# Kernel optimization log

Measured on AMD Instinct MI355X. Metric: run time of the kernel, lower is better.

## Reference

```python
import jax, jax.numpy as jnp
import numpy as np

TAU_PRE = 2.0
TAU_POST = 2.0
KH, KW = 3, 3
B, CIN, H, W = 16, 64, 66, 66
COUT = 128
HOUT, WOUT = H - KH + 1, W - KW + 1  # stride 1, padding 0


def setup_inputs() -> dict:
    key = jax.random.key(0)
    k1, k2, k3, k4, k5 = jax.random.split(key, 5)
    in_spike = jax.random.uniform(k1, (B, CIN, H, W), dtype=jnp.float32)
    out_spike = jax.random.uniform(k2, (B, COUT, HOUT, WOUT), dtype=jnp.float32)
    trace_pre = jax.random.uniform(k3, (B, CIN, H, W), dtype=jnp.float32)
    trace_post = jax.random.uniform(k4, (B, COUT, HOUT, WOUT), dtype=jnp.float32)
    weight = jax.random.normal(k5, (COUT, CIN, KH, KW), dtype=jnp.float32) * 0.05
    return {"in_spike": in_spike, "out_spike": out_spike,
            "trace_pre": trace_pre, "trace_post": trace_post, "weight": weight}


def reference(in_spike, out_spike, trace_pre, trace_post, weight):
    # Trace decay + spike accumulation (faithful to torch: tr - tr/tau + spike)
    tr_pre = trace_pre - trace_pre / TAU_PRE + in_spike    # [B,Cin,H,W]
    tr_post = trace_post - trace_post / TAU_POST + out_spike  # [B,Cout,Hout,Wout]

    rows = []
    for h in range(KH):
        cols = []
        for w in range(KW):
            pre = in_spike[:, :, h:h + HOUT, w:w + WOUT]   # [B,Cin,Hout,Wout]
            trp = tr_pre[:, :, h:h + HOUT, w:w + WOUT]     # [B,Cin,Hout,Wout]
            wk = weight[:, :, h, w]                        # [Cout,Cin]
            # sum over batch and spatial dims of outer products
            s_pre = jnp.einsum('bopq,bipq->oi', tr_post, pre)      # [Cout,Cin]
            s_post = jnp.einsum('bipq,bopq->oi', trp, out_spike)   # [Cout,Cin]
            cols.append(-wk * s_pre + wk * s_post)
        rows.append(jnp.stack(cols, axis=-1))  # [Cout,Cin,KW]
    delta_w = jnp.stack(rows, axis=-2)          # [Cout,Cin,KH,KW]
    return tr_pre, tr_post, delta_w
```

## Files before the change

### kernel.cpp

```cpp
#include <hip/hip_runtime.h>


typedef unsigned short ushort_t;
typedef unsigned int uint_t;
typedef __attribute__((ext_vector_type(8))) short short8;
typedef __attribute__((ext_vector_type(4))) float floatx4;
typedef __attribute__((ext_vector_type(2))) float floatx2;

#define N_PRE   4460544
#define N_POST  8388608
#define N_DW    73728
#define O_TRPOST 4460544
#define O_DW     12849152
#define BSLICE   4325376

#define GLDS16(g, l) __builtin_amdgcn_global_load_lds( \
    (const __attribute__((address_space(1))) void*)(g), \
    (__attribute__((address_space(3))) void*)(l), 16, 0, 0)

__device__ __forceinline__ ushort_t f2bf(float f) {
  uint_t u = __builtin_bit_cast(uint_t, f);
  u = (u + 0x7FFFu + ((u >> 16) & 1u)) >> 16;
  return (ushort_t)u;
}

__global__ void k_pre_elem(const float* __restrict__ in_sp, const float* __restrict__ tpre,
                           float* __restrict__ o_trpre) {
  int t4 = (blockIdx.x * 256 + threadIdx.x) * 4;
  floatx4 tp = *(const floatx4*)(tpre + t4);
  floatx4 is = *(const floatx4*)(in_sp + t4);
  *(floatx4*)(o_trpre + t4) = 0.5f * tp + is;
}

__global__ void k_bfill(const float* __restrict__ in_sp, const float* __restrict__ tpre,
                        ushort_t* __restrict__ B1, ushort_t* __restrict__ B2) {
  int tid = blockIdx.x * 256 + threadIdx.x;
  int row = tid >> 3, q8 = (tid & 7) * 8;
  int g = row * 66 + q8;
  float ftp[10], fin[10];
  #pragma unroll
  for (int k = 0; k < 5; ++k) {
    floatx2 a = *(const floatx2*)(tpre + g + 2 * k);
    floatx2 b = *(const floatx2*)(in_sp + g + 2 * k);
    ftp[2 * k] = a.x; ftp[2 * k + 1] = a.y;
    fin[2 * k] = b.x; fin[2 * k + 1] = b.y;
  }
  ushort_t utp[10], uin[10];
  #pragma unroll
  for (int k = 0; k < 10; ++k) { utp[k] = f2bf(ftp[k]); uin[k] = f2bf(fin[k]); }
  int dst = row * 64 + q8;
  #pragma unroll
  for (int kw = 0; kw < 3; ++kw) {
    short8 v1, v2;
    #pragma unroll
    for (int k = 0; k < 8; ++k) { v1[k] = (short)utp[kw + k]; v2[k] = (short)uin[kw + k]; }
    *(short8*)(B1 + kw * BSLICE + dst) = v1;
    *(short8*)(B2 + kw * BSLICE + dst) = v2;
  }
}

__global__ void k_post(const float* __restrict__ out_sp, const float* __restrict__ tpost,
                       float* __restrict__ o_trpost,
                       ushort_t* __restrict__ A1, ushort_t* __restrict__ A2, int write_ws) {
  int t8 = (blockIdx.x * 256 + threadIdx.x) * 8;
  floatx4 o0 = *(const floatx4*)(out_sp + t8);
  floatx4 o1 = *(const floatx4*)(out_sp + t8 + 4);
  floatx4 p0 = *(const floatx4*)(tpost + t8);
  floatx4 p1 = *(const floatx4*)(tpost + t8 + 4);
  *(floatx4*)(o_trpost + t8)     = 0.5f * p0 + o0;
  *(floatx4*)(o_trpost + t8 + 4) = 0.5f * p1 + o1;
  if (write_ws) {
    short8 va, vn;
    #pragma unroll
    for (int k = 0; k < 4; ++k) {
      va[k] = (short)f2bf(o0[k]); va[k + 4] = (short)f2bf(o1[k]);
      vn[k] = (short)f2bf(-p0[k]); vn[k + 4] = (short)f2bf(-p1[k]);
    }
    *(short8*)(A1 + t8) = va;
    *(short8*)(A2 + t8) = vn;
  }
}

__global__ __launch_bounds__(128, 3)
void k_mfma(const ushort_t* __restrict__ A1, const ushort_t* __restrict__ A2,
            const ushort_t* __restrict__ B1, const ushort_t* __restrict__ B2,
            float* __restrict__ partials) {
  __shared__ short LA[8192];
  __shared__ short LB[8192];

  const int oh = blockIdx.y, e = blockIdx.z;
  const int kh = e / 3, kw = e - kh * 3;
  const int t = threadIdx.x, w = t >> 6, l = t & 63;
  const int quad = l >> 4, l16 = l & 15;
  const int wo = w * 32;

  const int lrow = l >> 3;
  const int s_sw = (l & 7) ^ (lrow & 7);
  const int aoff_lane = lrow * 4096 + s_sw * 8;
  const int boff_lane = lrow * 4224 + s_sw * 8;

  const ushort_t* PA = (w == 0) ? A1 : A2;
  const ushort_t* PB = ((w == 0) ? B1 : B2) + kw * BSLICE;
  short* la = LA + w * 4096;
  short* lb = LB + w * 4096;

  floatx4 acc[2][4] = {};

  for (int rr = 0; rr < 16; ++rr) {
    const int r = blockIdx.x * 16 + rr;
    const int b = r >> 6, p = r & 63;
    const ushort_t* ga = PA + b * 524288 + oh * 262144 + p * 64 + aoff_lane;
    const ushort_t* gb = PB + b * 270336 + (p + kh) * 64 + boff_lane;

    __syncthreads();
    #pragma unroll
    for (int j = 0; j < 8; ++j) {
      GLDS16(ga + j * 32768, la + j * 512);
      GLDS16(gb + j * 33792, lb + j * 512);
    }
    __syncthreads();

    #pragma unroll
    for (int ks = 0; ks < 2; ++ks) {
      const int s0 = ks * 4 + quad;
      const int o0 = wo + l16, o1 = wo + 16 + l16;
      const int ca0 = (o0 * 8 + (s0 ^ (o0 & 7))) * 8;
      const int ca1 = (o1 * 8 + (s0 ^ (o1 & 7))) * 8;
      short8 a00 = *(const short8*)&LA[ca0];
      short8 a10 = *(const short8*)&LA[4096 + ca0];
      short8 a01 = *(const short8*)&LA[ca1];
      short8 a11 = *(const short8*)&LA[4096 + ca1];
      #pragma unroll
      for (int nt = 0; nt < 4; ++nt) {
        const int i = nt * 16 + l16;
        const int cb = (i * 8 + (s0 ^ (i & 7))) * 8;
        short8 b0 = *(const short8*)&LB[cb];
        short8 b1 = *(const short8*)&LB[4096 + cb];
        acc[0][nt] = __builtin_amdgcn_mfma_f32_16x16x32_bf16(a00, b0, acc[0][nt], 0, 0, 0);
        acc[0][nt] = __builtin_amdgcn_mfma_f32_16x16x32_bf16(a10, b1, acc[0][nt], 0, 0, 0);
        acc[1][nt] = __builtin_amdgcn_mfma_f32_16x16x32_bf16(a01, b0, acc[1][nt], 0, 0, 0);
        acc[1][nt] = __builtin_amdgcn_mfma_f32_16x16x32_bf16(a11, b1, acc[1][nt], 0, 0, 0);
      }
    }
  }

  float* slice = partials + (size_t)((e * 64 + blockIdx.x) * 2 + oh) * 4096;
  #pragma unroll
  for (int mt = 0; mt < 2; ++mt)
    #pragma unroll
    for (int nt = 0; nt < 4; ++nt)
      #pragma unroll
      for (int rg = 0; rg < 4; ++rg) {
        int o = wo + mt * 16 + quad * 4 + rg;
        int i = nt * 16 + l16;
        slice[o * 64 + i] = acc[mt][nt][rg];
      }
}

__global__ void k_finalize(const float* __restrict__ partials,
                           const float* __restrict__ weight, float* __restrict__ dw) {
  int tid = blockIdx.x * 256 + threadIdx.x;
  int e = tid >> 13, oi = tid & 8191;
  int o = oi >> 6, i = oi & 63;
  int ohh = o >> 6, ol = o & 63;
  const float* pp = partials + (size_t)e * 524288 + ohh * 4096 + ol * 64 + i;
  float s = 0.f;
  #pragma unroll 8
  for (int x = 0; x < 64; ++x) s += pp[x * 8192];
  int wi = (o * 64 + i) * 9 + e;
  dw[wi] = 0.5f * weight[wi] * s;
}

__global__ void k_naive(const float* __restrict__ out_sp, const float* __restrict__ tpost,
                        const float* __restrict__ tpre, const float* __restrict__ in_sp,
                        const float* __restrict__ weight, float* __restrict__ dw) {
  int tid = blockIdx.x * 256 + threadIdx.x;
  int e = tid >> 13, oi = tid & 8191;
  int o = oi >> 6, i = oi & 63;
  int kh = e / 3, kw = e - kh * 3;
  float acc = 0.f;
  for (int b = 0; b < 16; ++b)
    for (int p = 0; p < 64; ++p) {
      const float* ga = out_sp + ((b * 128 + o) * 64 + p) * 64;
      const float* gn = tpost + ((b * 128 + o) * 64 + p) * 64;
      const float* gb = tpre + ((b * 64 + i) * 66 + p + kh) * 66 + kw;
      const float* gm = in_sp + ((b * 64 + i) * 66 + p + kh) * 66 + kw;
      for (int q = 0; q < 64; ++q) acc += ga[q] * gb[q] - gn[q] * gm[q];
    }
  int wi = (o * 64 + i) * 9 + kh * 3 + kw;
  dw[wi] = 0.5f * weight[wi] * acc;
}

extern "C" void kernel_launch(void* const* d_in, const int* in_sizes, int n_in,
                              void* d_out, int out_size, void* d_ws, size_t ws_size,
                              hipStream_t stream) {
  const float* in_sp  = (const float*)d_in[0];
  const float* out_sp = (const float*)d_in[1];
  const float* tpre   = (const float*)d_in[2];
  const float* tpost  = (const float*)d_in[3];
  const float* weight = (const float*)d_in[4];
  float* out = (float*)d_out;
  float* o_trpre  = out;
  float* o_trpost = out + O_TRPOST;
  float* o_dw     = out + O_DW;

  const size_t WS_NEED = 104333312;
  const int use_mfma = (ws_size >= WS_NEED) ? 1 : 0;
  ushort_t* A1 = (ushort_t*)d_ws;
  ushort_t* A2 = A1 + 8388608;
  ushort_t* B1 = A2 + 8388608;
  ushort_t* B2 = B1 + 3 * BSLICE;
  float* partials = (float*)(B2 + 3 * BSLICE);

  k_pre_elem<<<N_PRE / 4 / 256, 256, 0, stream>>>(in_sp, tpre, o_trpre);
  k_post<<<N_POST / 8 / 256, 256, 0, stream>>>(out_sp, tpost, o_trpost, A1, A2, use_mfma);
  if (use_mfma) {
    k_bfill<<<540672 / 256, 256, 0, stream>>>(in_sp, tpre, B1, B2);
    dim3 g(64, 2, 9);
    k_mfma<<<g, 128, 0, stream>>>(A1, A2, B1, B2, partials);
    k_finalize<<<N_DW / 256, 256, 0, stream>>>(partials, weight, o_dw);
  } else {
    k_naive<<<N_DW / 256, 256, 0, stream>>>(out_sp, tpost, tpre, in_sp, weight, o_dw);
  }
}
```

Measured before the change: 216.1 us.

## Fuse elementwise fill kernels and restructure MFMA kernel to direct register loads

```diff
diff --git a/kernel.cpp b/kernel.cpp
--- a/kernel.cpp
+++ b/kernel.cpp
@@ -14,159 +14,162 @@
 #define O_DW     12849152
 #define BSLICE   4325376
 
-#define GLDS16(g, l) __builtin_amdgcn_global_load_lds( \
-    (const __attribute__((address_space(1))) void*)(g), \
-    (__attribute__((address_space(3))) void*)(l), 16, 0, 0)
-
 __device__ __forceinline__ ushort_t f2bf(float f) {
   uint_t u = __builtin_bit_cast(uint_t, f);
   u = (u + 0x7FFFu + ((u >> 16) & 1u)) >> 16;
   return (ushort_t)u;
 }
 
-__global__ void k_pre_elem(const float* __restrict__ in_sp, const float* __restrict__ tpre,
-                           float* __restrict__ o_trpre) {
-  int t4 = (blockIdx.x * 256 + threadIdx.x) * 4;
-  floatx4 tp = *(const floatx4*)(tpre + t4);
-  floatx4 is = *(const floatx4*)(in_sp + t4);
-  *(floatx4*)(o_trpre + t4) = 0.5f * tp + is;
-}
-
-__global__ void k_bfill(const float* __restrict__ in_sp, const float* __restrict__ tpre,
-                        ushort_t* __restrict__ B1, ushort_t* __restrict__ B2) {
-  int tid = blockIdx.x * 256 + threadIdx.x;
-  int row = tid >> 3, q8 = (tid & 7) * 8;
-  int g = row * 66 + q8;
-  float ftp[10], fin[10];
-  #pragma unroll
-  for (int k = 0; k < 5; ++k) {
-    floatx2 a = *(const floatx2*)(tpre + g + 2 * k);
-    floatx2 b = *(const floatx2*)(in_sp + g + 2 * k);
-    ftp[2 * k] = a.x; ftp[2 * k + 1] = a.y;
-    fin[2 * k] = b.x; fin[2 * k + 1] = b.y;
-  }
-  ushort_t utp[10], uin[10];
-  #pragma unroll
-  for (int k = 0; k < 10; ++k) { utp[k] = f2bf(ftp[k]); uin[k] = f2bf(fin[k]); }
-  int dst = row * 64 + q8;
-  #pragma unroll
-  for (int kw = 0; kw < 3; ++kw) {
-    short8 v1, v2;
-    #pragma unroll
-    for (int k = 0; k < 8; ++k) { v1[k] = (short)utp[kw + k]; v2[k] = (short)uin[kw + k]; }
-    *(short8*)(B1 + kw * BSLICE + dst) = v1;
-    *(short8*)(B2 + kw * BSLICE + dst) = v2;
-  }
-}
-
-__global__ void k_post(const float* __restrict__ out_sp, const float* __restrict__ tpost,
-                       float* __restrict__ o_trpost,
-                       ushort_t* __restrict__ A1, ushort_t* __restrict__ A2, int write_ws) {
-  int t8 = (blockIdx.x * 256 + threadIdx.x) * 8;
-  floatx4 o0 = *(const floatx4*)(out_sp + t8);
-  floatx4 o1 = *(const floatx4*)(out_sp + t8 + 4);
-  floatx4 p0 = *(const floatx4*)(tpost + t8);
-  floatx4 p1 = *(const floatx4*)(tpost + t8 + 4);
-  *(floatx4*)(o_trpost + t8)     = 0.5f * p0 + o0;
-  *(floatx4*)(o_trpost + t8 + 4) = 0.5f * p1 + o1;
-  if (write_ws) {
-    short8 va, vn;
+__global__ __launch_bounds__(256)
+void k_fill(const float* __restrict__ in_sp, const float* __restrict__ out_sp,
+            const float* __restrict__ tpre, const float* __restrict__ tpost,
+            float* __restrict__ o_trpre, float* __restrict__ o_trpost,
+            ushort_t* __restrict__ A1, ushort_t* __restrict__ A2,
+            ushort_t* __restrict__ B1, ushort_t* __restrict__ B2, int use_ws) {
+  int bx = blockIdx.x;
+  if (bx < 2112) {
+    int tid = bx * 256 + threadIdx.x;
+    int row = tid >> 3, q8 = (tid & 7) * 8;
+    int g = row * 66 + q8;
+    float ftp[10], fin[10];
+    #pragma unroll
+    for (int k = 0; k < 5; ++k) {
+      floatx2 a = *(const floatx2*)(tpre + g + 2 * k);
+      floatx2 b = *(const floatx2*)(in_sp + g + 2 * k);
+      ftp[2 * k] = a.x; ftp[2 * k + 1] = a.y;
+      fin[2 * k] = b.x; fin[2 * k + 1] = b.y;
+    }
     #pragma unroll
     for (int k = 0; k < 4; ++k) {
-      va[k] = (short)f2bf(o0[k]); va[k + 4] = (short)f2bf(o1[k]);
-      vn[k] = (short)f2bf(-p0[k]); vn[k + 4] = (short)f2bf(-p1[k]);
-    }
-    *(short8*)(A1 + t8) = va;
-    *(short8*)(A2 + t8) = vn;
-  }
-}
-
-__global__ __launch_bounds__(128, 3)
+      floatx2 v = { 0.5f * ftp[2 * k] + fin[2 * k], 0.5f * ftp[2 * k + 1] + fin[2 * k + 1] };
+      *(floatx2*)(o_trpre + g + 2 * k) = v;
+    }
+    if (q8 == 56) {
+      floatx2 v = { 0.5f * ftp[8] + fin[8], 0.5f * ftp[9] + fin[9] };
+      *(floatx2*)(o_trpre + row * 66 + 64) = v;
+    }
+    if (use_ws) {
+      ushort_t utp[10], uin[10];
+      #pragma unroll
+      for (int k = 0; k < 10; ++k) { utp[k] = f2bf(ftp[k]); uin[k] = f2bf(fin[k]); }
+      int dst = row * 64 + q8;
+      #pragma unroll
+      for (int kw = 0; kw < 3; ++kw) {
+        short8 v1, v2;
+        #pragma unroll
+        for (int k = 0; k < 8; ++k) { v1[k] = (short)utp[kw + k]; v2[k] = (short)uin[kw + k]; }
+        *(short8*)(B1 + kw * BSLICE + dst) = v1;
+        *(short8*)(B2 + kw * BSLICE + dst) = v2;
+      }
+    }
+  } else {
+    int t8 = ((bx - 2112) * 256 + threadIdx.x) * 8;
+    floatx4 o0 = *(const floatx4*)(out_sp + t8);
+    floatx4 o1 = *(const floatx4*)(out_sp + t8 + 4);
+    floatx4 p0 = *(const floatx4*)(tpost + t8);
+    floatx4 p1 = *(const floatx4*)(tpost + t8 + 4);
+    *(floatx4*)(o_trpost + t8)     = 0.5f * p0 + o0;
+    *(floatx4*)(o_trpost + t8 + 4) = 0.5f * p1 + o1;
+    if (use_ws) {
+      short8 va, vn;
+      #pragma unroll
+      for (int k = 0; k < 4; ++k) {
+        va[k] = (short)f2bf(o0[k]); va[k + 4] = (short)f2bf(o1[k]);
+        vn[k] = (short)f2bf(-p0[k]); vn[k + 4] = (short)f2bf(-p1[k]);
+      }
+      *(short8*)(A1 + t8) = va;
+      *(short8*)(A2 + t8) = vn;
+    }
+  }
+}
+
+__global__ __launch_bounds__(256, 3)
 void k_mfma(const ushort_t* __restrict__ A1, const ushort_t* __restrict__ A2,
             const ushort_t* __restrict__ B1, const ushort_t* __restrict__ B2,
             float* __restrict__ partials) {
-  __shared__ short LA[8192];
-  __shared__ short LB[8192];
-
-  const int oh = blockIdx.y, e = blockIdx.z;
-  const int kh = e / 3, kw = e - kh * 3;
+  __shared__ float LRED[2][4096];
+
+  const int e = blockIdx.y, kh = e / 3, kw = e - kh * 3;
+  const int bx = blockIdx.x;
   const int t = threadIdx.x, w = t >> 6, l = t & 63;
+  const int ksub = w >> 1, oh = w & 1;
   const int quad = l >> 4, l16 = l & 15;
-  const int wo = w * 32;
-
-  const int lrow = l >> 3;
-  const int s_sw = (l & 7) ^ (lrow & 7);
-  const int aoff_lane = lrow * 4096 + s_sw * 8;
-  const int boff_lane = lrow * 4224 + s_sw * 8;
-
-  const ushort_t* PA = (w == 0) ? A1 : A2;
-  const ushort_t* PB = ((w == 0) ? B1 : B2) + kw * BSLICE;
-  short* la = LA + w * 4096;
-  short* lb = LB + w * 4096;
-
-  floatx4 acc[2][4] = {};
-
-  for (int rr = 0; rr < 16; ++rr) {
-    const int r = blockIdx.x * 16 + rr;
-    const int b = r >> 6, p = r & 63;
-    const ushort_t* ga = PA + b * 524288 + oh * 262144 + p * 64 + aoff_lane;
-    const ushort_t* gb = PB + b * 270336 + (p + kh) * 64 + boff_lane;
-
-    __syncthreads();
-    #pragma unroll
-    for (int j = 0; j < 8; ++j) {
-      GLDS16(ga + j * 32768, la + j * 512);
-      GLDS16(gb + j * 33792, lb + j * 512);
-    }
-    __syncthreads();
-
-    #pragma unroll
-    for (int ks = 0; ks < 2; ++ks) {
-      const int s0 = ks * 4 + quad;
-      const int o0 = wo + l16, o1 = wo + 16 + l16;
-      const int ca0 = (o0 * 8 + (s0 ^ (o0 & 7))) * 8;
-      const int ca1 = (o1 * 8 + (s0 ^ (o1 & 7))) * 8;
-      short8 a00 = *(const short8*)&LA[ca0];
-      short8 a10 = *(const short8*)&LA[4096 + ca0];
-      short8 a01 = *(const short8*)&LA[ca1];
-      short8 a11 = *(const short8*)&LA[4096 + ca1];
-      #pragma unroll
-      for (int nt = 0; nt < 4; ++nt) {
-        const int i = nt * 16 + l16;
-        const int cb = (i * 8 + (s0 ^ (i & 7))) * 8;
-        short8 b0 = *(const short8*)&LB[cb];
-        short8 b1 = *(const short8*)&LB[4096 + cb];
-        acc[0][nt] = __builtin_amdgcn_mfma_f32_16x16x32_bf16(a00, b0, acc[0][nt], 0, 0, 0);
-        acc[0][nt] = __builtin_amdgcn_mfma_f32_16x16x32_bf16(a10, b1, acc[0][nt], 0, 0, 0);
-        acc[1][nt] = __builtin_amdgcn_mfma_f32_16x16x32_bf16(a01, b0, acc[1][nt], 0, 0, 0);
-        acc[1][nt] = __builtin_amdgcn_mfma_f32_16x16x32_bf16(a11, b1, acc[1][nt], 0, 0, 0);
-      }
-    }
-  }
-
-  float* slice = partials + (size_t)((e * 64 + blockIdx.x) * 2 + oh) * 4096;
-  #pragma unroll
-  for (int mt = 0; mt < 2; ++mt)
-    #pragma unroll
-    for (int nt = 0; nt < 4; ++nt)
-      #pragma unroll
-      for (int rg = 0; rg < 4; ++rg) {
-        int o = wo + mt * 16 + quad * 4 + rg;
-        int i = nt * 16 + l16;
-        slice[o * 64 + i] = acc[mt][nt][rg];
-      }
+  const int b = bx >> 2;
+  const int p0 = (bx & 3) * 16 + ksub * 8;
+
+  const ushort_t* pa1 = A1 + (size_t)b * 524288 + p0 * 64;
+  const ushort_t* pa2 = A2 + (size_t)b * 524288 + p0 * 64;
+  const ushort_t* pb1 = B1 + kw * BSLICE + (size_t)b * 270336 + (p0 + kh) * 64;
+  const ushort_t* pb2 = B2 + kw * BSLICE + (size_t)b * 270336 + (p0 + kh) * 64;
+
+  int aoff[4], boff[4];
+  #pragma unroll
+  for (int mt = 0; mt < 4; ++mt) aoff[mt] = (oh * 64 + mt * 16 + l16) * 4096 + quad * 8;
+  #pragma unroll
+  for (int it = 0; it < 4; ++it) boff[it] = (it * 16 + l16) * 4224 + quad * 8;
+
+  floatx4 acc[4][4] = {};
+  short8 fa[4], fb[4], ga[4], gb[4];
+
+  #pragma unroll
+  for (int mt = 0; mt < 4; ++mt) fa[mt] = *(const short8*)(pa1 + aoff[mt]);
+  #pragma unroll
+  for (int it = 0; it < 4; ++it) fb[it] = *(const short8*)(pb1 + boff[it]);
+
+  #pragma unroll
+  for (int hs = 0; hs < 32; ++hs) {
+    if (hs < 31) {
+      const int nh = hs + 1;
+      const int off = (nh >> 2) * 64 + ((nh >> 1) & 1) * 32;
+      const ushort_t* qa = (nh & 1) ? pa2 : pa1;
+      const ushort_t* qb = (nh & 1) ? pb2 : pb1;
+      #pragma unroll
+      for (int mt = 0; mt < 4; ++mt) ga[mt] = *(const short8*)(qa + aoff[mt] + off);
+      #pragma unroll
+      for (int it = 0; it < 4; ++it) gb[it] = *(const short8*)(qb + boff[it] + off);
+    }
+    #pragma unroll
+    for (int mt = 0; mt < 4; ++mt)
+      #pragma unroll
+      for (int it = 0; it < 4; ++it)
+        acc[mt][it] = __builtin_amdgcn_mfma_f32_16x16x32_bf16(fa[mt], fb[it], acc[mt][it], 0, 0, 0);
+    #pragma unroll
+    for (int x = 0; x < 4; ++x) { fa[x] = ga[x]; fb[x] = gb[x]; }
+  }
+
+  if (ksub == 1) {
+    #pragma unroll
+    for (int mt = 0; mt < 4; ++mt)
+      #pragma unroll
+      for (int it = 0; it < 4; ++it)
+        #pragma unroll
+        for (int rg = 0; rg < 4; ++rg)
+          LRED[oh][(mt * 16 + quad * 4 + rg) * 64 + it * 16 + l16] = acc[mt][it][rg];
+  }
+  __syncthreads();
+  if (ksub == 0) {
+    float* slice = partials + (size_t)(e * 64 + bx) * 8192;
+    #pragma unroll
+    for (int mt = 0; mt < 4; ++mt)
+      #pragma unroll
+      for (int it = 0; it < 4; ++it)
+        #pragma unroll
+        for (int rg = 0; rg < 4; ++rg) {
+          int ol = mt * 16 + quad * 4 + rg;
+          int i = it * 16 + l16;
+          slice[(oh * 64 + ol) * 64 + i] = acc[mt][it][rg] + LRED[oh][ol * 64 + i];
+        }
+  }
 }
 
 __global__ void k_finalize(const float* __restrict__ partials,
                            const float* __restrict__ weight, float* __restrict__ dw) {
   int tid = blockIdx.x * 256 + threadIdx.x;
   int e = tid >> 13, oi = tid & 8191;
-  int o = oi >> 6, i = oi & 63;
-  int ohh = o >> 6, ol = o & 63;
-  const float* pp = partials + (size_t)e * 524288 + ohh * 4096 + ol * 64 + i;
   float s = 0.f;
   #pragma unroll 8
-  for (int x = 0; x < 64; ++x) s += pp[x * 8192];
+  for (int c = 0; c < 64; ++c) s += partials[(size_t)(e * 64 + c) * 8192 + oi];
+  int o = oi >> 6, i = oi & 63;
   int wi = (o * 64 + i) * 9 + e;
   dw[wi] = 0.5f * weight[wi] * s;
 }
@@ -212,12 +215,11 @@
   ushort_t* B2 = B1 + 3 * BSLICE;
   float* partials = (float*)(B2 + 3 * BSLICE);
 
-  k_pre_elem<<<N_PRE / 4 / 256, 256, 0, stream>>>(in_sp, tpre, o_trpre);
-  k_post<<<N_POST / 8 / 256, 256, 0, stream>>>(out_sp, tpost, o_trpost, A1, A2, use_mfma);
+  k_fill<<<6208, 256, 0, stream>>>(in_sp, out_sp, tpre, tpost,
+                                   o_trpre, o_trpost, A1, A2, B1, B2, use_mfma);
   if (use_mfma) {
-    k_bfill<<<540672 / 256, 256, 0, stream>>>(in_sp, tpre, B1, B2);
-    dim3 g(64, 2, 9);
-    k_mfma<<<g, 128, 0, stream>>>(A1, A2, B1, B2, partials);
+    dim3 g(64, 9);
+    k_mfma<<<g, 256, 0, stream>>>(A1, A2, B1, B2, partials);
     k_finalize<<<N_DW / 256, 256, 0, stream>>>(partials, weight, o_dw);
   } else {
     k_naive<<<N_DW / 256, 256, 0, stream>>>(out_sp, tpost, tpre, in_sp, weight, o_dw);
```

After: 250.8 us. 1.16x slower.
